# Optimization experiments

Measured on AMD Instinct MI355X. Metric: run time of the kernel, lower is better.

The kernel has to match this reference:

```python
import jax, jax.numpy as jnp
import numpy as np

DIM = 48
HEADS = 4
DIM_HEAD = 16
WS = 800  # window_size
INNER = HEADS * DIM_HEAD  # 64
SCALE = DIM_HEAD ** -0.5


def setup_inputs() -> dict:
    key = jax.random.key(0)
    k1, k2, k3, k4, k5 = jax.random.split(key, 5)
    b, n = 4, 6400
    x1 = jax.random.normal(k1, (b, n, DIM), dtype=jnp.float32)
    x2 = jax.random.normal(k2, (b, n, DIM), dtype=jnp.float32)
    # to_qkv: Linear(dim, inner*3, bias=False) -> weight [3*inner, dim] (torch layout)
    Wqkv = jax.random.normal(k3, (3 * INNER, DIM), dtype=jnp.float32) * (DIM ** -0.5)
    # to_out: Linear(inner, dim) with bias (project_out is True since heads=4, dim_head=16 != dim)
    Wout = jax.random.normal(k4, (DIM, INNER), dtype=jnp.float32) * (INNER ** -0.5)
    bout = jax.random.normal(k5, (DIM,), dtype=jnp.float32) * 0.01
    return {"x1": x1, "x2": x2, "Wqkv": Wqkv, "Wout": Wout, "bout": bout}


def _windowed_attn(x, Wqkv):
    # x: [b, n, c] with n divisible by WS -> independent full attention per window
    b, n, c = x.shape
    nw = n // WS
    xw = x.reshape(b, nw, WS, c)
    # Rearrange 'b n (head dim_head)' with head=HEADS on 3*inner dim, then chunk(3)
    # => layout along last axis is (heads, 3, dim_head)
    qkv = jnp.einsum('bwic,oc->bwio', xw, Wqkv).reshape(b, nw, WS, HEADS, 3, DIM_HEAD)
    q, k, v = qkv[..., 0, :], qkv[..., 1, :], qkv[..., 2, :]  # [b,nw,ws,h,dh]
    dots = jnp.einsum('bwihd,bwjhd->bwhij', q, k) * SCALE      # [b,nw,h,ws,ws]
    attn = jax.nn.softmax(dots, axis=-1)
    out = jnp.einsum('bwhij,bwjhd->bwihd', attn, v)            # [b,nw,ws,h,dh]
    return out.reshape(b, n, INNER)


def reference(x1, x2, Wqkv, Wout, bout):
    o1 = _windowed_attn(x1, Wqkv) @ Wout.T + bout
    o2 = _windowed_attn(x2, Wqkv) @ Wout.T + bout
    return o1 + o2
```

## Files before the change

### kernel.cpp

```cpp
#include <hip/hip_runtime.h>
#include <cstddef>

typedef __attribute__((ext_vector_type(8))) short short8;
typedef __attribute__((ext_vector_type(16))) float f32x16;

#define NB 4
#define NSEQ 6400
#define CDIM 48
#define DHEAD 16
#define WSZ 800
#define NWIN 8
#define INNER 64
#define NROWS 25600
#define NWH 256
#define SCHUNK (WSZ * DHEAD)
#define CHUNK (3 * SCHUNK)
#define QKV_TOTAL (NWH * CHUNK)
#define AO_PER (NROWS * INNER)

static __device__ __forceinline__ uint pkbf(float a, float b) {
  uint r;
  asm("v_cvt_pk_bf16_f32 %0, %1, %2" : "=v"(r) : "v"(a), "v"(b));
  return r;
}

__global__ __launch_bounds__(256) void qkv_mfma(const float* __restrict__ x1,
                                                const float* __restrict__ x2,
                                                const float* __restrict__ Wqkv,
                                                ushort* __restrict__ wsq) {
  const int tid = threadIdx.x;
  const int lane = tid & 63;
  const int wv = tid >> 6;

  __shared__ __align__(16) ushort Wl[18 * 64 * 8];
  __shared__ __align__(16) ushort Obuf[4][6 * 512];

  for (int slot = tid; slot < 1152; slot += 256) {
    const int mtks = slot >> 6, l2 = slot & 63;
    const int mt = mtks / 3, ks = mtks % 3;
    const int o = mt * 32 + (l2 & 31);
    const int c0 = ks * 16 + (l2 >> 5) * 8;
    const float sc = ((o % CDIM) < DHEAD) ? 0.25f : 1.0f;
    const float4* p = reinterpret_cast<const float4*>(Wqkv + (size_t)o * CDIM + c0);
    float4 u = p[0], v = p[1];
    union { uint q[4]; short8 s; } t;
    t.q[0] = pkbf(u.x * sc, u.y * sc); t.q[1] = pkbf(u.z * sc, u.w * sc);
    t.q[2] = pkbf(v.x * sc, v.y * sc); t.q[3] = pkbf(v.z * sc, v.w * sc);
    *reinterpret_cast<short8*>(Wl + (size_t)slot * 8) = t.s;
  }
  __syncthreads();

  const int task = blockIdx.x * 4 + wv;
  const int batch = task >> 1;
  const int mh = task & 1;
  const int e = batch / 800;
  const int rb = (batch % 800) * 32;
  const float* __restrict__ x = e ? x2 : x1;

  const int rl = lane & 31;
  const int lg = lane >> 5;
  const int row = rb + rl;

  short8 bf[3];
#pragma unroll
  for (int ks = 0; ks < 3; ++ks) {
    const float4* p =
        reinterpret_cast<const float4*>(x + (size_t)row * CDIM + ks * 16 + lg * 8);
    float4 u = p[0], v = p[1];
    union { uint q[4]; short8 s; } t;
    t.q[0] = pkbf(u.x, u.y); t.q[1] = pkbf(u.z, u.w);
    t.q[2] = pkbf(v.x, v.y); t.q[3] = pkbf(v.z, v.w);
    bf[ks] = t.s;
  }

  const int b = rb / NSEQ;
  const int i0 = rb % NSEQ;
  const int wi = i0 / WSZ;
  const int iwb = i0 % WSZ;
  const int whb = ((e * NB + b) * NWIN + wi) * 4;

#pragma unroll
  for (int mt = mh * 3; mt < mh * 3 + 3; ++mt) {
    const int obase = mt * 32;
    short8 wf0 = *reinterpret_cast<const short8*>(Wl + ((mt * 3 + 0) * 64 + lane) * 8);
    short8 wf1 = *reinterpret_cast<const short8*>(Wl + ((mt * 3 + 1) * 64 + lane) * 8);
    short8 wf2 = *reinterpret_cast<const short8*>(Wl + ((mt * 3 + 2) * 64 + lane) * 8);

    f32x16 acc;
#pragma unroll
    for (int r = 0; r < 16; ++r) acc[r] = 0.f;
    acc = __builtin_amdgcn_mfma_f32_32x32x16_bf16(wf0, bf[0], acc, 0, 0, 0);
    acc = __builtin_amdgcn_mfma_f32_32x32x16_bf16(wf1, bf[1], acc, 0, 0, 0);
    acc = __builtin_amdgcn_mfma_f32_32x32x16_bf16(wf2, bf[2], acc, 0, 0, 0);

#pragma unroll
    for (int q = 0; q < 4; ++q) {
      const int op = obase + q * 8 + 4 * lg - mh * 96;
      const int g2 = op >> 4;
      const int d0 = op & 15;
      uint2 pk;
      pk.x = pkbf(acc[4 * q + 0], acc[4 * q + 1]);
      pk.y = pkbf(acc[4 * q + 2], acc[4 * q + 3]);
      *reinterpret_cast<uint2*>(&Obuf[wv][g2 * 512 + rl * 16 + d0]) = pk;
    }
  }

#pragma unroll
  for (int g2 = 0; g2 < 6; ++g2) {
    const int g = mh * 6 + g2;
    const int h = g / 3, s = g % 3;
    short8 val = *reinterpret_cast<const short8*>(&Obuf[wv][g2 * 512 + lane * 8]);
    *reinterpret_cast<short8*>(wsq + (size_t)(whb + h) * CHUNK + s * SCHUNK +
                               (size_t)iwb * DHEAD + lane * 8) = val;
  }
}

#define JC 160
#define NCH 5
#define KSL (5 * 64 * 8)
#define VROW 168
#define VSL (17 * VROW)

__global__ __launch_bounds__(320) void attn_mfma(const ushort* __restrict__ wsq,
                                                 float* __restrict__ ao) {
  const int tid = threadIdx.x;
  const int lane = tid & 63;
  const int wv = tid >> 6;
  const int bid = blockIdx.x;
  const int wh = bid & (NWH - 1);
  const int sub = bid >> 8;
  const int qtile = sub * 5 + wv;

  const ushort* __restrict__ Qg = wsq + (size_t)wh * CHUNK;
  const ushort* __restrict__ Kg = Qg + SCHUNK;
  const ushort* __restrict__ Vg = Kg + SCHUNK;

  __shared__ __align__(16) ushort Ks[2][KSL];
  __shared__ __align__(16) ushort Vs[2][VSL];

  const int kj = (tid >> 6) * 32 + (tid & 31);
  const int khalf = (tid >> 5) & 1;
  const int vj = tid % 160;
  const int vhalf = tid / 160;

  short8 kreg = *reinterpret_cast<const short8*>(Kg + (size_t)kj * DHEAD + khalf * 8);
  short8 vreg = *reinterpret_cast<const short8*>(Vg + (size_t)vj * DHEAD + vhalf * 8);

  if (tid < JC) {
    Vs[0][16 * VROW + tid] = 0x3F80;
    Vs[1][16 * VROW + tid] = 0x3F80;
  }

  *reinterpret_cast<short8*>(&Ks[0][tid * 8]) = kreg;
#pragma unroll
  for (int u = 0; u < 8; ++u)
    Vs[0][(vhalf * 8 + u) * VROW + vj] = (ushort)vreg[u];

  kreg = *reinterpret_cast<const short8*>(Kg + (size_t)(JC + kj) * DHEAD + khalf * 8);
  vreg = *reinterpret_cast<const short8*>(Vg + (size_t)(JC + vj) * DHEAD + vhalf * 8);

  short8 qf = *reinterpret_cast<const short8*>(
      Qg + (size_t)(qtile * 32 + (lane & 31)) * DHEAD + (lane >> 5) * 8);

  __syncthreads();

  f32x16 sinit;
#pragma unroll
  for (int r = 0; r < 16; ++r) sinit[r] = -8.0f;
  f32x16 accO;
#pragma unroll
  for (int r = 0; r < 16; ++r) accO[r] = 0.f;

  const int n31 = lane & 31;
  const int lg = lane >> 5;
  const int vrow = (n31 <= 16) ? n31 : (n31 & 15);

  for (int ch = 0; ch < NCH; ++ch) {
    const ushort* __restrict__ Kc = Ks[ch & 1];
    const ushort* __restrict__ Vc = Vs[ch & 1];
#pragma unroll
    for (int jl = 0; jl < 5; ++jl) {
      short8 kf = *reinterpret_cast<const short8*>(Kc + (jl * 64 + lane) * 8);
      f32x16 st = __builtin_amdgcn_mfma_f32_32x32x16_bf16(kf, qf, sinit, 0, 0, 0);

      float p[16];
#pragma unroll
      for (int r = 0; r < 16; ++r) p[r] = __expf(st[r]);

      uint x0, x1, y0, y1;
      asm("v_cvt_pk_bf16_f32 %0, %1, %2" : "=v"(x0) : "v"(p[0]), "v"(p[1]));
      asm("v_cvt_pk_bf16_f32 %0, %1, %2" : "=v"(x1) : "v"(p[2]), "v"(p[3]));
      asm("v_cvt_pk_bf16_f32 %0, %1, %2" : "=v"(y0) : "v"(p[4]), "v"(p[5]));
      asm("v_cvt_pk_bf16_f32 %0, %1, %2" : "=v"(y1) : "v"(p[6]), "v"(p[7]));
      asm("v_permlane32_swap_b32 %0, %1" : "+v"(x0), "+v"(y0));
      asm("v_permlane32_swap_b32 %0, %1" : "+v"(x1), "+v"(y1));
      union { uint u[4]; short8 s; } pa0;
      pa0.u[0] = x0; pa0.u[1] = x1; pa0.u[2] = y0; pa0.u[3] = y1;

      uint z0, z1, w0, w1;
      asm("v_cvt_pk_bf16_f32 %0, %1, %2" : "=v"(z0) : "v"(p[8]), "v"(p[9]));
      asm("v_cvt_pk_bf16_f32 %0, %1, %2" : "=v"(z1) : "v"(p[10]), "v"(p[11]));
      asm("v_cvt_pk_bf16_f32 %0, %1, %2" : "=v"(w0) : "v"(p[12]), "v"(p[13]));
      asm("v_cvt_pk_bf16_f32 %0, %1, %2" : "=v"(w1) : "v"(p[14]), "v"(p[15]));
      asm("v_permlane32_swap_b32 %0, %1" : "+v"(z0), "+v"(w0));
      asm("v_permlane32_swap_b32 %0, %1" : "+v"(z1), "+v"(w1));
      union { uint u[4]; short8 s; } pa1;
      pa1.u[0] = z0; pa1.u[1] = z1; pa1.u[2] = w0; pa1.u[3] = w1;

      short8 vf0 = *reinterpret_cast<const short8*>(Vc + vrow * VROW + jl * 32 + lg * 8);
      short8 vf1 = *reinterpret_cast<const short8*>(Vc + vrow * VROW + jl * 32 + 16 + lg * 8);

      accO = __builtin_amdgcn_mfma_f32_32x32x16_bf16(pa0.s, vf0, accO, 0, 0, 0);
      accO = __builtin_amdgcn_mfma_f32_32x32x16_bf16(pa1.s, vf1, accO, 0, 0, 0);
    }
    if (ch + 1 < NCH) {
      __syncthreads();
      const int nxt = (ch + 1) & 1;
      *reinterpret_cast<short8*>(&Ks[nxt][tid * 8]) = kreg;
#pragma unroll
      for (int u = 0; u < 8; ++u)
        Vs[nxt][(vhalf * 8 + u) * VROW + vj] = (ushort)vreg[u];
      if (ch + 2 < NCH) {
        kreg = *reinterpret_cast<const short8*>(
            Kg + (size_t)((ch + 2) * JC + kj) * DHEAD + khalf * 8);
        vreg = *reinterpret_cast<const short8*>(
            Vg + (size_t)((ch + 2) * JC + vj) * DHEAD + vhalf * 8);
      }
      __syncthreads();
    }
  }

  const int h = wh & 3;
  const int w = (wh >> 2) & 7;
  const int b = (wh >> 5) & 3;
  const int e = wh >> 7;
  const size_t rowbase =
      (size_t)e * NROWS + (size_t)b * NSEQ + (size_t)w * WSZ + (size_t)qtile * 32;
  const int src = 16 + 32 * lg;

#pragma unroll
  for (int r = 0; r < 16; ++r) {
    float den = __shfl(accO[r], src);
    if (n31 < 16) {
      int i = (r & 3) + 8 * (r >> 2) + 4 * lg;
      ao[(rowbase + i) * INNER + h * DHEAD + n31] =
          accO[r] * __builtin_amdgcn_rcpf(den);
    }
  }
}

#define OSTR 76
__global__ __launch_bounds__(192) void out_proj(const float* __restrict__ ao_all,
                                                const float* __restrict__ Wout,
                                                const float* __restrict__ bout,
                                                float* __restrict__ out) {
  const int tid = threadIdx.x;
  const int row0 = blockIdx.x * 64;

  __shared__ float aos[64 * OSTR];

  const float4* __restrict__ a14 = reinterpret_cast<const float4*>(ao_all);
  const float4* __restrict__ a24 = a14 + (size_t)NROWS * (INNER / 4);

  for (int idx = tid; idx < 64 * 16; idx += 192) {
    const int r = idx >> 4, k4 = idx & 15;
    float4 u = a14[(size_t)(row0 + r) * 16 + k4];
    float4 v = a24[(size_t)(row0 + r) * 16 + k4];
    float4 s;
    s.x = u.x + v.x; s.y = u.y + v.y; s.z = u.z + v.z; s.w = u.w + v.w;
    *reinterpret_cast<float4*>(aos + r * OSTR + k4 * 4) = s;
  }

  const int j = tid % 48;
  const int rq = tid / 48;

  float wreg[INNER];
#pragma unroll
  for (int k4 = 0; k4 < 16; ++k4) {
    float4 wv4 = reinterpret_cast<const float4*>(Wout + (size_t)j * INNER)[k4];
    wreg[k4 * 4 + 0] = wv4.x; wreg[k4 * 4 + 1] = wv4.y;
    wreg[k4 * 4 + 2] = wv4.z; wreg[k4 * 4 + 3] = wv4.w;
  }
  const float bj = 2.0f * bout[j];

  __syncthreads();

  for (int r16 = 0; r16 < 16; ++r16) {
    const int r = rq * 16 + r16;
    float a0 = 0.f, a1 = 0.f, a2 = 0.f, a3 = 0.f;
#pragma unroll
    for (int kk = 0; kk < 16; ++kk) {
      const int k4 = (kk + rq * 4) & 15;
      float4 av = *reinterpret_cast<const float4*>(aos + r * OSTR + k4 * 4);
      a0 = fmaf(av.x, wreg[k4 * 4 + 0], a0);
      a1 = fmaf(av.y, wreg[k4 * 4 + 1], a1);
      a2 = fmaf(av.z, wreg[k4 * 4 + 2], a2);
      a3 = fmaf(av.w, wreg[k4 * 4 + 3], a3);
    }
    out[(size_t)(row0 + r) * CDIM + j] = (a0 + a1) + (a2 + a3) + bj;
  }
}

extern "C" void kernel_launch(void* const* d_in, const int* in_sizes, int n_in,
                              void* d_out, int out_size, void* d_ws,
                              size_t ws_size, hipStream_t stream) {
  const float* x1 = (const float*)d_in[0];
  const float* x2 = (const float*)d_in[1];
  const float* Wqkv = (const float*)d_in[2];
  const float* Wout = (const float*)d_in[3];
  const float* bout = (const float*)d_in[4];
  float* out = (float*)d_out;
  ushort* wsq = (ushort*)d_ws;
  float* ao = (float*)(wsq + QKV_TOTAL);

  qkv_mfma<<<dim3(800), dim3(256), 0, stream>>>(x1, x2, Wqkv, wsq);
  attn_mfma<<<dim3(1280), dim3(320), 0, stream>>>(wsq, ao);
  out_proj<<<dim3(400), dim3(192), 0, stream>>>(ao, Wout, bout, out);
}
```

Measured before the change: 66.38 us.

## Read K fragments directly from global and store attention output as bf16

Removes the shared-memory staging and double-buffering of K in the attention kernel, so each lane loads its K fragment straight from global memory (expected to hit in cache). The attention output buffer is also changed from fp32 to bf16, roughly halving the intermediate write and the read in out_proj, which now converts back to float on load. This trades LDS traffic for repeated global or L2 loads of K, and lowers the precision of the intermediate attention output.

```diff
diff --git a/kernel.cpp b/kernel.cpp
--- a/kernel.cpp
+++ b/kernel.cpp
@@ -23,6 +23,9 @@
   asm("v_cvt_pk_bf16_f32 %0, %1, %2" : "=v"(r) : "v"(a), "v"(b));
   return r;
 }
+static __device__ __forceinline__ float bf2f(ushort u) {
+  return __uint_as_float(((uint)u) << 16);
+}
 
 __global__ __launch_bounds__(256) void qkv_mfma(const float* __restrict__ x1,
                                                 const float* __restrict__ x2,
@@ -117,12 +120,11 @@
 
 #define JC 160
 #define NCH 5
-#define KSL (5 * 64 * 8)
 #define VROW 168
 #define VSL (17 * VROW)
 
 __global__ __launch_bounds__(320) void attn_mfma(const ushort* __restrict__ wsq,
-                                                 float* __restrict__ ao) {
+                                                 ushort* __restrict__ ao) {
   const int tid = threadIdx.x;
   const int lane = tid & 63;
   const int wv = tid >> 6;
@@ -135,15 +137,11 @@
   const ushort* __restrict__ Kg = Qg + SCHUNK;
   const ushort* __restrict__ Vg = Kg + SCHUNK;
 
-  __shared__ __align__(16) ushort Ks[2][KSL];
   __shared__ __align__(16) ushort Vs[2][VSL];
 
-  const int kj = (tid >> 6) * 32 + (tid & 31);
-  const int khalf = (tid >> 5) & 1;
   const int vj = tid % 160;
   const int vhalf = tid / 160;
 
-  short8 kreg = *reinterpret_cast<const short8*>(Kg + (size_t)kj * DHEAD + khalf * 8);
   short8 vreg = *reinterpret_cast<const short8*>(Vg + (size_t)vj * DHEAD + vhalf * 8);
 
   if (tid < JC) {
@@ -151,12 +149,10 @@
     Vs[1][16 * VROW + tid] = 0x3F80;
   }
 
-  *reinterpret_cast<short8*>(&Ks[0][tid * 8]) = kreg;
 #pragma unroll
   for (int u = 0; u < 8; ++u)
     Vs[0][(vhalf * 8 + u) * VROW + vj] = (ushort)vreg[u];
 
-  kreg = *reinterpret_cast<const short8*>(Kg + (size_t)(JC + kj) * DHEAD + khalf * 8);
   vreg = *reinterpret_cast<const short8*>(Vg + (size_t)(JC + vj) * DHEAD + vhalf * 8);
 
   short8 qf = *reinterpret_cast<const short8*>(
@@ -174,13 +170,14 @@
   const int n31 = lane & 31;
   const int lg = lane >> 5;
   const int vrow = (n31 <= 16) ? n31 : (n31 & 15);
+  const ushort* __restrict__ kfb = Kg + (size_t)n31 * DHEAD + lg * 8;
 
   for (int ch = 0; ch < NCH; ++ch) {
-    const ushort* __restrict__ Kc = Ks[ch & 1];
     const ushort* __restrict__ Vc = Vs[ch & 1];
 #pragma unroll
     for (int jl = 0; jl < 5; ++jl) {
-      short8 kf = *reinterpret_cast<const short8*>(Kc + (jl * 64 + lane) * 8);
+      short8 kf = *reinterpret_cast<const short8*>(
+          kfb + (size_t)(ch * JC + jl * 32) * DHEAD);
       f32x16 st = __builtin_amdgcn_mfma_f32_32x32x16_bf16(kf, qf, sinit, 0, 0, 0);
 
       float p[16];
@@ -216,13 +213,10 @@
     if (ch + 1 < NCH) {
       __syncthreads();
       const int nxt = (ch + 1) & 1;
-      *reinterpret_cast<short8*>(&Ks[nxt][tid * 8]) = kreg;
 #pragma unroll
       for (int u = 0; u < 8; ++u)
         Vs[nxt][(vhalf * 8 + u) * VROW + vj] = (ushort)vreg[u];
       if (ch + 2 < NCH) {
-        kreg = *reinterpret_cast<const short8*>(
-            Kg + (size_t)((ch + 2) * JC + kj) * DHEAD + khalf * 8);
         vreg = *reinterpret_cast<const short8*>(
             Vg + (size_t)((ch + 2) * JC + vj) * DHEAD + vhalf * 8);
       }
@@ -243,14 +237,14 @@
     float den = __shfl(accO[r], src);
     if (n31 < 16) {
       int i = (r & 3) + 8 * (r >> 2) + 4 * lg;
-      ao[(rowbase + i) * INNER + h * DHEAD + n31] =
-          accO[r] * __builtin_amdgcn_rcpf(den);
+      float val = accO[r] * __builtin_amdgcn_rcpf(den);
+      ao[(rowbase + i) * INNER + h * DHEAD + n31] = (ushort)pkbf(val, val);
     }
   }
 }
 
 #define OSTR 76
-__global__ __launch_bounds__(192) void out_proj(const float* __restrict__ ao_all,
+__global__ __launch_bounds__(192) void out_proj(const ushort* __restrict__ ao_all,
                                                 const float* __restrict__ Wout,
                                                 const float* __restrict__ bout,
                                                 float* __restrict__ out) {
@@ -259,16 +253,25 @@
 
   __shared__ float aos[64 * OSTR];
 
-  const float4* __restrict__ a14 = reinterpret_cast<const float4*>(ao_all);
-  const float4* __restrict__ a24 = a14 + (size_t)NROWS * (INNER / 4);
-
-  for (int idx = tid; idx < 64 * 16; idx += 192) {
-    const int r = idx >> 4, k4 = idx & 15;
-    float4 u = a14[(size_t)(row0 + r) * 16 + k4];
-    float4 v = a24[(size_t)(row0 + r) * 16 + k4];
-    float4 s;
-    s.x = u.x + v.x; s.y = u.y + v.y; s.z = u.z + v.z; s.w = u.w + v.w;
-    *reinterpret_cast<float4*>(aos + r * OSTR + k4 * 4) = s;
+  const ushort* __restrict__ a1 = ao_all;
+  const ushort* __restrict__ a2 = ao_all + (size_t)AO_PER;
+
+  for (int idx = tid; idx < 64 * 8; idx += 192) {
+    const int r = idx >> 3, c = idx & 7;
+    const size_t g = (size_t)(row0 + r) * INNER + c * 8;
+    short8 u = *reinterpret_cast<const short8*>(a1 + g);
+    short8 v = *reinterpret_cast<const short8*>(a2 + g);
+    float4 s0, s1;
+    s0.x = bf2f((ushort)u[0]) + bf2f((ushort)v[0]);
+    s0.y = bf2f((ushort)u[1]) + bf2f((ushort)v[1]);
+    s0.z = bf2f((ushort)u[2]) + bf2f((ushort)v[2]);
+    s0.w = bf2f((ushort)u[3]) + bf2f((ushort)v[3]);
+    s1.x = bf2f((ushort)u[4]) + bf2f((ushort)v[4]);
+    s1.y = bf2f((ushort)u[5]) + bf2f((ushort)v[5]);
+    s1.z = bf2f((ushort)u[6]) + bf2f((ushort)v[6]);
+    s1.w = bf2f((ushort)u[7]) + bf2f((ushort)v[7]);
+    *reinterpret_cast<float4*>(aos + r * OSTR + c * 8) = s0;
+    *reinterpret_cast<float4*>(aos + r * OSTR + c * 8 + 4) = s1;
   }
 
   const int j = tid % 48;
@@ -287,17 +290,17 @@
 
   for (int r16 = 0; r16 < 16; ++r16) {
     const int r = rq * 16 + r16;
-    float a0 = 0.f, a1 = 0.f, a2 = 0.f, a3 = 0.f;
+    float a0 = 0.f, a1v = 0.f, a2v = 0.f, a3 = 0.f;
 #pragma unroll
     for (int kk = 0; kk < 16; ++kk) {
       const int k4 = (kk + rq * 4) & 15;
       float4 av = *reinterpret_cast<const float4*>(aos + r * OSTR + k4 * 4);
       a0 = fmaf(av.x, wreg[k4 * 4 + 0], a0);
-      a1 = fmaf(av.y, wreg[k4 * 4 + 1], a1);
-      a2 = fmaf(av.z, wreg[k4 * 4 + 2], a2);
+      a1v = fmaf(av.y, wreg[k4 * 4 + 1], a1v);
+      a2v = fmaf(av.z, wreg[k4 * 4 + 2], a2v);
       a3 = fmaf(av.w, wreg[k4 * 4 + 3], a3);
     }
-    out[(size_t)(row0 + r) * CDIM + j] = (a0 + a1) + (a2 + a3) + bj;
+    out[(size_t)(row0 + r) * CDIM + j] = (a0 + a1v) + (a2v + a3) + bj;
   }
 }
 
@@ -311,7 +314,7 @@
   const float* bout = (const float*)d_in[4];
   float* out = (float*)d_out;
   ushort* wsq = (ushort*)d_ws;
-  float* ao = (float*)(wsq + QKV_TOTAL);
+  ushort* ao = wsq + QKV_TOTAL;
 
   qkv_mfma<<<dim3(800), dim3(256), 0, stream>>>(x1, x2, Wqkv, wsq);
   attn_mfma<<<dim3(1280), dim3(320), 0, stream>>>(wsq, ao);
```

Measured after the change: 65.74 us, median of 2. Within noise of the previous version (-1.0%).
